# Performance work log

Measured on AMD Instinct MI355X. Metric: run time of the kernel, lower is better.

## Reference

```python
import jax, jax.numpy as jnp
import numpy as np
import math

B, S, H, NH, R = 1, 1024, 4096, 32, 16
HD = H // NH
BLOCK = 64
PRUNE_RATIO = 0.5
NF4_TABLE = jnp.array([
    -1.0, -0.6961928009986877, -0.5250730514526367, -0.39491748809814453,
    -0.28444138169288635, -0.18477343022823334, -0.09105003625154495, 0.0,
    0.07958029955625534, 0.16093020141124725, 0.24611230194568634,
    0.33791524171829224, 0.4407098591327667, 0.5626170039176941,
    0.7229568362236023, 1.0], dtype=jnp.float32)


def dequant_nf4(codes, absmax):
    # codes: [out,in] int4 values in [0,16); absmax: per-64-elem block scale
    vals = NF4_TABLE[codes.reshape(-1)]                 # [out*in]
    vals = vals.reshape(-1, BLOCK) * absmax[:, None]    # blockwise rescale
    return vals.reshape(codes.shape)                    # [out,in]


def setup_inputs() -> dict:
    key = jax.random.key(0)
    ks = jax.random.split(key, 32)
    d = {"x": jax.random.normal(ks[0], (B, S, H), dtype=jnp.float32)}
    i = 1
    for n in ("q", "k", "v", "o"):
        d[f"w_{n}_codes"] = jax.random.randint(ks[i], (H, H), 0, 16, dtype=jnp.int32); i += 1
        d[f"w_{n}_absmax"] = jax.random.uniform(ks[i], (H * H // BLOCK,), dtype=jnp.float32) * 0.06; i += 1
        d[f"b_{n}"] = jax.random.normal(ks[i], (H,), dtype=jnp.float32) * 0.01; i += 1
        d[f"w_{n}_lora_a"] = jax.random.normal(ks[i], (H, R), dtype=jnp.float32) * (1.0 / math.sqrt(H)); i += 1
        d[f"w_{n}_lora_b"] = jax.random.normal(ks[i], (R, H), dtype=jnp.float32) * 0.02; i += 1
    causal = jnp.tril(jnp.ones((S, S), dtype=bool))
    d["attention_mask"] = jnp.where(causal, 0.0, -1e9).astype(jnp.float32)[None, None]
    return d


def _proj(x, codes, absmax, b, la, lb):
    w = dequant_nf4(codes, absmax).T          # [in,out]
    main = x @ w + b
    lora_a = x @ la                            # [B,S,R]
    return main + lora_a @ lb, main, lora_a


def _kth_val(t, use_abs=True):
    flat = jnp.abs(t).ravel() if use_abs else t.ravel()
    k = int(t.size * PRUNE_RATIO)
    return jnp.sort(flat)[k - 1]


def reference(x, w_q_codes, w_q_absmax, b_q, w_q_lora_a, w_q_lora_b,
              w_k_codes, w_k_absmax, b_k, w_k_lora_a, w_k_lora_b,
              w_v_codes, w_v_absmax, b_v, w_v_lora_a, w_v_lora_b,
              w_o_codes, w_o_absmax, b_o, w_o_lora_a, w_o_lora_b,
              attention_mask):
    q, _, _ = _proj(x, w_q_codes, w_q_absmax, b_q, w_q_lora_a, w_q_lora_b)
    k, _, _ = _proj(x, w_k_codes, w_k_absmax, b_k, w_k_lora_a, w_k_lora_b)
    v, _, _ = _proj(x, w_v_codes, w_v_absmax, b_v, w_v_lora_a, w_v_lora_b)
    # [B,S,H] -> [B,NH,S,HD]
    qh = q.reshape(B, S, NH, HD).transpose(0, 2, 1, 3)
    kh = k.reshape(B, S, NH, HD).transpose(0, 2, 1, 3)
    vh = v.reshape(B, S, NH, HD).transpose(0, 2, 1, 3)
    s = jnp.einsum("bhqd,bhkd->bhqk", qh, kh) / math.sqrt(HD) + attention_mask
    a = jax.nn.softmax(s, axis=-1)
    o = jnp.einsum("bhqk,bhkd->bhqd", a, vh)
    o = o.transpose(0, 2, 1, 3).reshape(B, S, H)
    o_final, _, _ = _proj(o, w_o_codes, w_o_absmax, b_o, w_o_lora_a, w_o_lora_b)
    # iteration < 10 branch: magnitude-pruning thresholds via kth smallest value
    kth_vals = jnp.stack([
        _kth_val(x), _kth_val(qh), _kth_val(kh), _kth_val(vh),
        _kth_val(a, use_abs=False), _kth_val(o)])
    return o_final, kth_vals
```

## Files before the change

### kernel.cpp

```cpp
#include <hip/hip_runtime.h>

#define S_LEN  1024
#define H_DIM  4096
#define NHEAD  32
#define HEAD_D 128
#define RANK   16
#define KE3    4160
#define KEO    4128
#define TOTP   ((long)NHEAD * S_LEN * S_LEN)

typedef __bf16 bf16x8 __attribute__((ext_vector_type(8)));
typedef float  f32x4  __attribute__((ext_vector_type(4)));
typedef unsigned short ushort8v __attribute__((ext_vector_type(8)));

#define GLOAD_LDS16(g, l) __builtin_amdgcn_global_load_lds( \
    (const __attribute__((address_space(1))) unsigned int*)(g), \
    (__attribute__((address_space(3))) unsigned int*)(l), 16, 0, 0)

__device__ const float NF4_TAB[16] = {
    -1.0f, -0.6961928009986877f, -0.5250730514526367f, -0.39491748809814453f,
    -0.28444138169288635f, -0.18477343022823334f, -0.09105003625154495f, 0.0f,
    0.07958029955625534f, 0.16093020141124725f, 0.24611230194568634f,
    0.33791524171829224f, 0.4407098591327667f, 0.5626170039176941f,
    0.7229568362236023f, 1.0f};

__device__ __forceinline__ unsigned short f2bf(float f) {
    unsigned int u = __builtin_bit_cast(unsigned int, f);
    u = (u + 0x7FFFu + ((u >> 16) & 1u)) >> 16;
    return (unsigned short)u;
}

__device__ __forceinline__ float bf2f(unsigned short s) {
    return __builtin_bit_cast(float, (unsigned int)s << 16);
}

__device__ __forceinline__ void dequant_body(
    const int* __restrict__ codes, const float* __restrict__ absmax,
    unsigned short* __restrict__ out, long i, int ostride) {
    int4 c0 = *(const int4*)(codes + i);
    int4 c1 = *(const int4*)(codes + i + 4);
    float am = absmax[i >> 6];
    long orow = i >> 12;
    int  col  = (int)(i & 4095);
    ushort8v r;
    r[0] = f2bf(NF4_TAB[c0.x] * am);
    r[1] = f2bf(NF4_TAB[c0.y] * am);
    r[2] = f2bf(NF4_TAB[c0.z] * am);
    r[3] = f2bf(NF4_TAB[c0.w] * am);
    r[4] = f2bf(NF4_TAB[c1.x] * am);
    r[5] = f2bf(NF4_TAB[c1.y] * am);
    r[6] = f2bf(NF4_TAB[c1.z] * am);
    r[7] = f2bf(NF4_TAB[c1.w] * am);
    *(ushort8v*)(out + orow * ostride + col) = r;
}

__global__ __launch_bounds__(256) void prep_weights(
    const int* __restrict__ c0, const int* __restrict__ c1,
    const int* __restrict__ c2, const int* __restrict__ c3,
    const float* __restrict__ a0, const float* __restrict__ a1,
    const float* __restrict__ a2, const float* __restrict__ a3,
    const float* __restrict__ lb0, const float* __restrict__ lb1,
    const float* __restrict__ lb2, const float* __restrict__ lb3,
    const float* __restrict__ b0, const float* __restrict__ b1,
    const float* __restrict__ b2,
    unsigned short* __restrict__ wqkv, unsigned short* __restrict__ wo,
    float* __restrict__ bias3, unsigned int* __restrict__ hist, long n) {
    int p = blockIdx.y;
    long bx = blockIdx.x;
    int tid = threadIdx.x;
    if (bx < 8192) {
        const int* codes = (p == 0) ? c0 : (p == 1) ? c1 : (p == 2) ? c2 : c3;
        const float* am  = (p == 0) ? a0 : (p == 1) ? a1 : (p == 2) ? a2 : a3;
        long i = (bx * 256 + tid) * 8;
        if (i >= n) return;
        if (p < 3) dequant_body(codes, am, wqkv + (size_t)p * H_DIM * KE3, i, KE3);
        else       dequant_body(codes, am, wo, i, KEO);
        return;
    }
    if (p < 3) {
        long g = (bx - 8192) * 256 + tid;
        int row = (int)(g >> 6), c = (int)(g & 63);
        const float* lb = (p == 0) ? lb0 : (p == 1) ? lb1 : lb2;
        unsigned int r = (unsigned int)(c - 16 * p);
        float v = (r < 16u) ? lb[r * H_DIM + row] : 0.f;
        wqkv[(size_t)p * H_DIM * KE3 + (long)row * KE3 + 4096 + c] = f2bf(v);
        if (g < H_DIM) {
            const float* bp = (p == 0) ? b0 : (p == 1) ? b1 : b2;
            bias3[(size_t)p * H_DIM + g] = bp[g];
        }
        return;
    }
    if (bx < 8704) {
        long g = (bx - 8192) * 256 + tid;
        if (g >= (long)H_DIM * 32) return;
        int row = (int)(g >> 5), c = (int)(g & 31);
        float v = (c < 16) ? lb3[c * H_DIM + row] : 0.f;
        wo[(long)row * KEO + 4096 + c] = f2bf(v);
        return;
    }
    if (bx < 9088) {
        long g = (bx - 8704) * 256 + tid;
        if (g < 6 * 16384) hist[g] = 0u;
    }
}

__global__ __launch_bounds__(256) void cast_lora(
    const float* __restrict__ x, const float* __restrict__ la0,
    const float* __restrict__ la1, const float* __restrict__ la2,
    unsigned short* __restrict__ xb_ext) {
    __shared__ float xs[4096];
    int m = blockIdx.x, tid = threadIdx.x;
    const float* xr = x + (long)m * H_DIM;
    int c = tid * 16;
    float4 f0 = *(const float4*)(xr + c);
    float4 f1 = *(const float4*)(xr + c + 4);
    float4 f2 = *(const float4*)(xr + c + 8);
    float4 f3 = *(const float4*)(xr + c + 12);
    *(float4*)(xs + c)      = f0;
    *(float4*)(xs + c + 4)  = f1;
    *(float4*)(xs + c + 8)  = f2;
    *(float4*)(xs + c + 12) = f3;
    ushort8v r0, r1;
    r0[0] = f2bf(f0.x); r0[1] = f2bf(f0.y); r0[2] = f2bf(f0.z); r0[3] = f2bf(f0.w);
    r0[4] = f2bf(f1.x); r0[5] = f2bf(f1.y); r0[6] = f2bf(f1.z); r0[7] = f2bf(f1.w);
    r1[0] = f2bf(f2.x); r1[1] = f2bf(f2.y); r1[2] = f2bf(f2.z); r1[3] = f2bf(f2.w);
    r1[4] = f2bf(f3.x); r1[5] = f2bf(f3.y); r1[6] = f2bf(f3.z); r1[7] = f2bf(f3.w);
    unsigned short* orow = xb_ext + (long)m * KE3 + c;
    *(ushort8v*)orow = r0;
    *(ushort8v*)(orow + 8) = r1;
    __syncthreads();
    int w = tid >> 6, lane = tid & 63;
    if (w < 3) {
        const float* la = (w == 0) ? la0 : (w == 1) ? la1 : la2;
        float s[16];
#pragma unroll
        for (int r = 0; r < 16; ++r) s[r] = 0.f;
        for (int k = lane; k < H_DIM; k += 64) {
            float xv = xs[k];
            const float4* lr = (const float4*)(la + (long)k * RANK);
            float4 q0 = lr[0], q1 = lr[1], q2 = lr[2], q3 = lr[3];
            s[0] += xv * q0.x;  s[1] += xv * q0.y;  s[2] += xv * q0.z;  s[3] += xv * q0.w;
            s[4] += xv * q1.x;  s[5] += xv * q1.y;  s[6] += xv * q1.z;  s[7] += xv * q1.w;
            s[8] += xv * q2.x;  s[9] += xv * q2.y;  s[10] += xv * q2.z; s[11] += xv * q2.w;
            s[12] += xv * q3.x; s[13] += xv * q3.y; s[14] += xv * q3.z; s[15] += xv * q3.w;
        }
        for (int off = 32; off; off >>= 1)
#pragma unroll
            for (int r = 0; r < 16; ++r) s[r] += __shfl_xor(s[r], off);
        if (lane == 0)
#pragma unroll
            for (int r = 0; r < 16; ++r)
                xb_ext[(long)m * KE3 + 4096 + 16 * w + r] = f2bf(s[r]);
    }
}

__global__ void transpose_bf16_kernel(const unsigned short* __restrict__ v,
                                      unsigned short* __restrict__ vt) {
    __shared__ unsigned short tile[32][33];
    int c0 = blockIdx.x * 32, s0 = blockIdx.y * 32;
    int tx = threadIdx.x, ty = threadIdx.y;
    tile[ty][tx] = v[(long)(s0 + ty) * H_DIM + c0 + tx];
    __syncthreads();
    vt[(long)(c0 + ty) * S_LEN + s0 + tx] = tile[tx][ty];
}

__global__ __launch_bounds__(256) void lora_ao_kernel(
    unsigned short* __restrict__ ob_ext, const float* __restrict__ la) {
    int m = blockIdx.x;
    const unsigned short* xr = ob_ext + (long)m * KEO;
    int tid = threadIdx.x, lane = tid & 63, wid = tid >> 6;
    float s[4] = {0.f, 0.f, 0.f, 0.f};
    for (int k = lane; k < H_DIM; k += 64) {
        float xv = bf2f(xr[k]);
        const float* lr = la + (long)k * RANK + wid * 4;
        s[0] += xv * lr[0]; s[1] += xv * lr[1];
        s[2] += xv * lr[2]; s[3] += xv * lr[3];
    }
    for (int off = 32; off; off >>= 1)
        for (int r = 0; r < 4; ++r) s[r] += __shfl_down(s[r], off);
    if (lane == 0)
        for (int r = 0; r < 4; ++r)
            ob_ext[(long)m * KEO + 4096 + wid * 4 + r] = f2bf(s[r]);
}

__global__ __launch_bounds__(256) void gemm_nt(
    const unsigned short* __restrict__ A, const unsigned short* __restrict__ B,
    void* __restrict__ Cv, void* __restrict__ Cv2, const float* __restrict__ bias,
    int K, int lda, int ldb, int ldc,
    long strideA, long strideB, long strideC, float alpha, int mode, int obf) {
    int bm, bn;
    int k0s = 0, k0e = K;
    if (mode == 1) {
        int i = blockIdx.x;
        int tm = (int)((sqrtf(8.f * i + 1.f) - 1.f) * 0.5f);
        if ((tm + 1) * (tm + 2) / 2 <= i) tm++;
        if (tm * (tm + 1) / 2 > i) tm--;
        int tn = i - tm * (tm + 1) / 2;
        bm = tm * 128; bn = tn * 128;
    } else {
        bm = blockIdx.y * 128; bn = blockIdx.x * 128;
        if (mode == 2) { int kl = bm + 128; if (kl < k0e) k0e = kl; }
    }
    const unsigned short* Ab = A;
    const unsigned short* Bb = B;
    long coff = 0;
    void* Cuse = Cv;
    if (mode == 3) {
        int Kh = (K / 2) & ~31;
        k0s = blockIdx.z ? Kh : 0;
        k0e = blockIdx.z ? K : Kh;
        Cuse = blockIdx.z ? Cv2 : Cv;
    } else {
        Ab += (long)blockIdx.z * strideA;
        Bb += (long)blockIdx.z * strideB;
        coff = (long)blockIdx.z * strideC;
    }
    __shared__ unsigned short As[128][32];
    __shared__ unsigned short Bs[128][32];
    const int tid = threadIdx.x;
    const int lane = tid & 63, wid = tid >> 6;
    const int wm = (wid >> 1) * 64, wn = (wid & 1) * 64;
    const int sr = wid * 16 + (lane >> 2);
    const int sc = (lane & 3) * 8;
    const unsigned short* gA0 = Ab + (long)(bm + sr) * lda + sc;
    const unsigned short* gA1 = gA0 + (long)64 * lda;
    const unsigned short* gB0 = Bb + (long)(bn + sr) * ldb + sc;
    const unsigned short* gB1 = gB0 + (long)64 * ldb;
    unsigned short* lA0 = &As[wid * 16][0];
    unsigned short* lA1 = &As[64 + wid * 16][0];
    unsigned short* lB0 = &Bs[wid * 16][0];
    unsigned short* lB1 = &Bs[64 + wid * 16][0];
    f32x4 acc[4][4] = {};
    const int kq = (lane >> 4) * 8;
    const int rr = lane & 15;
    for (int k0 = k0s; k0 < k0e; k0 += 32) {
        GLOAD_LDS16(gA0 + k0, lA0);
        GLOAD_LDS16(gA1 + k0, lA1);
        GLOAD_LDS16(gB0 + k0, lB0);
        GLOAD_LDS16(gB1 + k0, lB1);
        __syncthreads();
        bf16x8 af[4], bfr[4];
        for (int i = 0; i < 4; ++i) {
            uint4 ta = *(const uint4*)&As[wm + i * 16 + rr][kq];
            uint4 tb = *(const uint4*)&Bs[wn + i * 16 + rr][kq];
            af[i]  = __builtin_bit_cast(bf16x8, ta);
            bfr[i] = __builtin_bit_cast(bf16x8, tb);
        }
        for (int i = 0; i < 4; ++i)
            for (int j = 0; j < 4; ++j)
                acc[i][j] = __builtin_amdgcn_mfma_f32_16x16x32_bf16(
                    af[i], bfr[j], acc[i][j], 0, 0, 0);
        __syncthreads();
    }
    const int cr = (lane >> 4) * 4;
    const int cc = lane & 15;
    float bv[4];
#pragma unroll
    for (int j = 0; j < 4; ++j)
        bv[j] = bias ? bias[(long)blockIdx.z * H_DIM + bn + wn + j * 16 + cc] : 0.f;
    if (obf) {
        unsigned short* Cb = (unsigned short*)Cuse + coff;
        for (int i = 0; i < 4; ++i)
            for (int j = 0; j < 4; ++j) {
                unsigned short* cp = Cb + (long)(bm + wm + i * 16 + cr) * ldc
                                        + (bn + wn + j * 16 + cc);
                for (int r = 0; r < 4; ++r)
                    cp[(long)r * ldc] = f2bf(acc[i][j][r] * alpha + bv[j]);
            }
    } else {
        float* Cb = (float*)Cuse + coff;
        for (int i = 0; i < 4; ++i)
            for (int j = 0; j < 4; ++j) {
                float* cp = Cb + (long)(bm + wm + i * 16 + cr) * ldc
                               + (bn + wn + j * 16 + cc);
                for (int r = 0; r < 4; ++r)
                    cp[(long)r * ldc] = acc[i][j][r] * alpha + bv[j];
            }
    }
}

__global__ __launch_bounds__(256) void combine_kernel(
    float* __restrict__ out, const float* __restrict__ part,
    const float* __restrict__ bias) {
    long idx = ((long)blockIdx.x * 256 + threadIdx.x) * 4;
    int n = (int)(idx & 4095);
    float4 o = *(float4*)(out + idx);
    float4 p = *(const float4*)(part + idx);
    float4 b = *(const float4*)(bias + n);
    o.x += p.x + b.x; o.y += p.y + b.y; o.z += p.z + b.z; o.w += p.w + b.w;
    *(float4*)(out + idx) = o;
}

__global__ __launch_bounds__(256) void softmax_causal(unsigned short* __restrict__ scores16) {
    int b = blockIdx.x;
    int h = b >> 9, pr = b & 511;
    int tid = threadIdx.x, lane = tid & 63, wid = tid >> 6;
    __shared__ float red[4], red2[4];
    for (int half = 0; half < 2; ++half) {
        int i = half ? (S_LEN - 1 - pr) : pr;
        unsigned short* row = scores16 + ((long)h * S_LEN + i) * S_LEN;
        int L = i + 1;
        float v[4];
        float mx = -1e30f;
        for (int t = 0; t < 4; ++t) {
            int j = tid + (t << 8);
            v[t] = (j < L) ? bf2f(row[j]) : -1e30f;
            mx = fmaxf(mx, v[t]);
        }
        for (int off = 32; off; off >>= 1) mx = fmaxf(mx, __shfl_xor(mx, off));
        if (lane == 0) red[wid] = mx;
        __syncthreads();
        mx = fmaxf(fmaxf(red[0], red[1]), fmaxf(red[2], red[3]));
        float e[4], sum = 0.f;
        for (int t = 0; t < 4; ++t) {
            int j = tid + (t << 8);
            e[t] = (j < L) ? __expf(v[t] - mx) : 0.f;
            sum += e[t];
        }
        for (int off = 32; off; off >>= 1) sum += __shfl_xor(sum, off);
        if (lane == 0) red2[wid] = sum;
        __syncthreads();
        sum = red2[0] + red2[1] + red2[2] + red2[3];
        float inv = 1.f / sum;
        for (int t = 0; t < 4; ++t) {
            int j = tid + (t << 8);
            row[j] = f2bf(e[t] * inv);
        }
        __syncthreads();
    }
}

__global__ __launch_bounds__(256, 2) void hist6(
    const float* __restrict__ x, const unsigned short* __restrict__ qkv,
    const unsigned short* __restrict__ ob, const unsigned short* __restrict__ P,
    unsigned int* __restrict__ hist) {
    __shared__ unsigned int lh[16384];
    const long SH = (long)S_LEN * H_DIM;
    int t = threadIdx.x;
    int b = blockIdx.x;
    int ten, b0, nblk;
    if (b < 256)      { ten = 0; b0 = 0;   nblk = 256; }
    else if (b < 384) { ten = 1; b0 = 256; nblk = 128; }
    else if (b < 512) { ten = 2; b0 = 384; nblk = 128; }
    else if (b < 640) { ten = 3; b0 = 512; nblk = 128; }
    else if (b < 768) { ten = 4; b0 = 640; nblk = 128; }
    else              { ten = 5; b0 = 768; nblk = 768; }
    unsigned int* gh = hist + (long)ten * 16384;
    for (int k = t; k < 16384; k += 256) lh[k] = 0u;
    __syncthreads();
    long i = (long)(b - b0) * 256 + t;
    long stride = (long)nblk * 256;
    if (ten == 0) {
        for (; i < SH / 4; i += stride) {
            float4 v = *(const float4*)(x + i * 4);
            unsigned int u0 = (__builtin_bit_cast(unsigned int, v.x) & 0x7FFFFFFFu) >> 16;
            unsigned int u1 = (__builtin_bit_cast(unsigned int, v.y) & 0x7FFFFFFFu) >> 16;
            unsigned int u2 = (__builtin_bit_cast(unsigned int, v.z) & 0x7FFFFFFFu) >> 16;
            unsigned int u3 = (__builtin_bit_cast(unsigned int, v.w) & 0x7FFFFFFFu) >> 16;
            atomicAdd(&lh[u0 < 16384u ? u0 : 16383u], 1u);
            atomicAdd(&lh[u1 < 16384u ? u1 : 16383u], 1u);
            atomicAdd(&lh[u2 < 16384u ? u2 : 16383u], 1u);
            atomicAdd(&lh[u3 < 16384u ? u3 : 16383u], 1u);
        }
    } else if (ten <= 3) {
        const unsigned short* src = qkv + (size_t)(ten - 1) * SH;
        for (; i < SH / 8; i += stride) {
            ushort8v v = ((const ushort8v*)src)[i];
#pragma unroll
            for (int j = 0; j < 8; ++j) {
                unsigned int u = v[j] & 0x7FFFu;
                atomicAdd(&lh[u < 16384u ? u : 16383u], 1u);
            }
        }
    } else if (ten == 4) {
        for (; i < SH / 8; i += stride) {
            long off = (i >> 9) * KEO + ((i & 511) << 3);
            ushort8v v = *(const ushort8v*)(ob + off);
#pragma unroll
            for (int j = 0; j < 8; ++j) {
                unsigned int u = v[j] & 0x7FFFu;
                atomicAdd(&lh[u < 16384u ? u : 16383u], 1u);
            }
        }
    } else {
        unsigned int zc = 0;
        for (; i < TOTP / 8; i += stride) {
            ushort8v v = ((const ushort8v*)P)[i];
#pragma unroll
            for (int j = 0; j < 8; ++j) {
                unsigned int bb = v[j];
                if (bb == 0) zc++;
                else atomicAdd(&lh[bb < 16384u ? bb : 16383u], 1u);
            }
        }
        if (zc) atomicAdd(&lh[0], zc);
    }
    __syncthreads();
    for (int k = t; k < 16384; k += 256) {
        unsigned int c = lh[k];
        if (c) atomicAdd(&gh[k], c);
    }
}

__global__ __launch_bounds__(256) void scan6(
    const unsigned int* __restrict__ hist, float* __restrict__ out_kth) {
    int ten = blockIdx.x;
    const unsigned int* h = hist + (long)ten * 16384;
    __shared__ unsigned int part[256];
    int t = threadIdx.x;
    unsigned int s = 0;
    for (int b = 0; b < 64; ++b) s += h[t * 64 + b];
    part[t] = s;
    __syncthreads();
    if (t == 0) {
        long k = (ten == 5) ? TOTP / 2 : (long)S_LEN * H_DIM / 2;
        long c = 0;
        int ch = 0;
        for (; ch < 256; ++ch) {
            if (c + (long)part[ch] >= k) break;
            c += part[ch];
        }
        int bin = ch * 64;
        for (;; ++bin) {
            unsigned int hv = h[bin];
            if (c + (long)hv >= k) break;
            c += hv;
        }
        int slot = (ten == 4) ? 5 : (ten == 5) ? 4 : ten;
        out_kth[slot] = __builtin_bit_cast(float, (unsigned int)bin << 16);
    }
}

extern "C" void kernel_launch(void* const* d_in, const int* in_sizes, int n_in,
                              void* d_out, int out_size, void* d_ws, size_t ws_size,
                              hipStream_t stream) {
    (void)in_sizes; (void)n_in; (void)out_size; (void)ws_size;
    const float* x = (const float*)d_in[0];
    const int*   wcodes[4] = {(const int*)d_in[1], (const int*)d_in[6],
                              (const int*)d_in[11], (const int*)d_in[16]};
    const float* wabs[4]   = {(const float*)d_in[2], (const float*)d_in[7],
                              (const float*)d_in[12], (const float*)d_in[17]};
    const float* bias[4]   = {(const float*)d_in[3], (const float*)d_in[8],
                              (const float*)d_in[13], (const float*)d_in[18]};
    const float* lA[4]     = {(const float*)d_in[4], (const float*)d_in[9],
                              (const float*)d_in[14], (const float*)d_in[19]};
    const float* lB[4]     = {(const float*)d_in[5], (const float*)d_in[10],
                              (const float*)d_in[15], (const float*)d_in[20]};

    char* wp = (char*)d_ws;
    auto alloc = [&](size_t bytes) {
        char* p = wp; wp += (bytes + 255) & ~(size_t)255; return p;
    };
    const size_t SH  = (size_t)S_LEN * H_DIM;
    const long   nW  = (long)H_DIM * H_DIM;
    unsigned short* xb_ext = (unsigned short*)alloc((size_t)S_LEN * KE3 * 2);
    unsigned short* qkvb   = (unsigned short*)alloc(3 * SH * 2);
    unsigned short* vT     = (unsigned short*)alloc(SH * 2);
    unsigned short* ob_ext = (unsigned short*)alloc((size_t)S_LEN * KEO * 2);
    unsigned short* Wd_ext = (unsigned short*)alloc((size_t)H_DIM * KEO * 2);
    float*        opart  = (float*)alloc(SH * 4);
    float*        bias3  = (float*)alloc(3 * H_DIM * 4);
    unsigned int* hist   = (unsigned int*)alloc(6 * 16384 * 4);
    char* bigbuf = alloc((size_t)3 * H_DIM * KE3 * 2);
    unsigned short* Wqkv_ext = (unsigned short*)bigbuf;
    unsigned short* scores16 = (unsigned short*)bigbuf;

    float* out_final = (float*)d_out;
    float* out_kth   = out_final + SH;

    unsigned short* qb = qkvb;
    unsigned short* kb = qkvb + SH;
    unsigned short* vb = qkvb + 2 * SH;

    prep_weights<<<dim3(9216, 4), 256, 0, stream>>>(
        wcodes[0], wcodes[1], wcodes[2], wcodes[3],
        wabs[0], wabs[1], wabs[2], wabs[3],
        lB[0], lB[1], lB[2], lB[3],
        bias[0], bias[1], bias[2],
        Wqkv_ext, Wd_ext, bias3, hist, nW);

    cast_lora<<<S_LEN, 256, 0, stream>>>(x, lA[0], lA[1], lA[2], xb_ext);

    gemm_nt<<<dim3(32, 8, 3), 256, 0, stream>>>(
        xb_ext, Wqkv_ext, qkvb, nullptr, bias3, KE3, KE3, KE3, H_DIM,
        0, (long)H_DIM * KE3, (long)SH, 1.0f, 0, 1);

    transpose_bf16_kernel<<<dim3(H_DIM / 32, S_LEN / 32), dim3(32, 32), 0, stream>>>(vb, vT);

    gemm_nt<<<dim3(36, 1, NHEAD), 256, 0, stream>>>(
        qb, kb, scores16, nullptr, nullptr, HEAD_D, H_DIM, H_DIM, S_LEN,
        128, 128, (long)S_LEN * S_LEN, 0.08838834764831845f, 1, 1);

    softmax_causal<<<NHEAD * S_LEN / 2, 256, 0, stream>>>(scores16);

    gemm_nt<<<dim3(1, 8, NHEAD), 256, 0, stream>>>(
        scores16, vT, ob_ext, nullptr, nullptr, S_LEN,
        S_LEN, S_LEN, KEO,
        (long)S_LEN * S_LEN, (long)HEAD_D * S_LEN, 128, 1.0f, 2, 1);

    lora_ao_kernel<<<S_LEN, 256, 0, stream>>>(ob_ext, lA[3]);

    gemm_nt<<<dim3(32, 8, 2), 256, 0, stream>>>(
        ob_ext, Wd_ext, out_final, opart, nullptr, KEO, KEO, KEO, H_DIM,
        0, 0, 0, 1.0f, 3, 0);

    combine_kernel<<<4096, 256, 0, stream>>>(out_final, opart, bias[3]);

    hist6<<<1536, 256, 0, stream>>>(x, qkvb, ob_ext, scores16, hist);
    scan6<<<6, 256, 0, stream>>>(hist, out_kth);
}
```

Measured before the change: 779.3 us.

## Fold V transpose into QK gemm, merge combine with scan, swap grid order

The standalone V transpose now runs inside the QK^T score gemm launch, in extra blocks (blockIdx.x >= 36) that tile-transpose V through shared memory while the other blocks compute scores. The combine and scan kernels become one finish kernel, and the gemm grid is reordered so blockIdx.x walks M tiles, which changes the block rasterisation and L2 reuse of weight tiles. The goal is fewer launches and some overlap of the transpose with score computation. The risk is that a few transpose blocks with 32 tiles each become stragglers in the attention gemm.

```diff
diff --git a/kernel.cpp b/kernel.cpp
--- a/kernel.cpp
+++ b/kernel.cpp
@@ -154,16 +154,6 @@
     }
 }
 
-__global__ void transpose_bf16_kernel(const unsigned short* __restrict__ v,
-                                      unsigned short* __restrict__ vt) {
-    __shared__ unsigned short tile[32][33];
-    int c0 = blockIdx.x * 32, s0 = blockIdx.y * 32;
-    int tx = threadIdx.x, ty = threadIdx.y;
-    tile[ty][tx] = v[(long)(s0 + ty) * H_DIM + c0 + tx];
-    __syncthreads();
-    vt[(long)(c0 + ty) * S_LEN + s0 + tx] = tile[tx][ty];
-}
-
 __global__ __launch_bounds__(256) void lora_ao_kernel(
     unsigned short* __restrict__ ob_ext, const float* __restrict__ la) {
     int m = blockIdx.x;
@@ -187,18 +177,38 @@
     const unsigned short* __restrict__ A, const unsigned short* __restrict__ B,
     void* __restrict__ Cv, void* __restrict__ Cv2, const float* __restrict__ bias,
     int K, int lda, int ldb, int ldc,
-    long strideA, long strideB, long strideC, float alpha, int mode, int obf) {
+    long strideA, long strideB, long strideC, float alpha, int mode, int obf,
+    const unsigned short* __restrict__ tsrc, unsigned short* __restrict__ tdst) {
+    __shared__ unsigned short As[128][32];
+    __shared__ unsigned short Bs[128][32];
+    const int tid = threadIdx.x;
     int bm, bn;
     int k0s = 0, k0e = K;
     if (mode == 1) {
         int i = blockIdx.x;
+        if (i >= 36) {
+            unsigned short (*tl)[33] = (unsigned short(*)[33])&As[0][0];
+            int tb = (i - 36) + 4 * blockIdx.z;
+            int tx = tid & 31, ty = tid >> 5;
+            for (int tile = tb; tile < 4096; tile += 128) {
+                int tc = tile & 127, ts = tile >> 7;
+                int c0 = tc * 32, s0 = ts * 32;
+                for (int j = 0; j < 32; j += 8)
+                    tl[ty + j][tx] = tsrc[(long)(s0 + ty + j) * H_DIM + c0 + tx];
+                __syncthreads();
+                for (int j = 0; j < 32; j += 8)
+                    tdst[(long)(c0 + ty + j) * S_LEN + s0 + tx] = tl[tx][ty + j];
+                __syncthreads();
+            }
+            return;
+        }
         int tm = (int)((sqrtf(8.f * i + 1.f) - 1.f) * 0.5f);
         if ((tm + 1) * (tm + 2) / 2 <= i) tm++;
         if (tm * (tm + 1) / 2 > i) tm--;
         int tn = i - tm * (tm + 1) / 2;
         bm = tm * 128; bn = tn * 128;
     } else {
-        bm = blockIdx.y * 128; bn = blockIdx.x * 128;
+        bm = blockIdx.x * 128; bn = blockIdx.y * 128;
         if (mode == 2) { int kl = bm + 128; if (kl < k0e) k0e = kl; }
     }
     const unsigned short* Ab = A;
@@ -215,9 +225,6 @@
         Bb += (long)blockIdx.z * strideB;
         coff = (long)blockIdx.z * strideC;
     }
-    __shared__ unsigned short As[128][32];
-    __shared__ unsigned short Bs[128][32];
-    const int tid = threadIdx.x;
     const int lane = tid & 63, wid = tid >> 6;
     const int wm = (wid >> 1) * 64, wn = (wid & 1) * 64;
     const int sr = wid * 16 + (lane >> 2);
@@ -277,18 +284,6 @@
                     cp[(long)r * ldc] = acc[i][j][r] * alpha + bv[j];
             }
     }
-}
-
-__global__ __launch_bounds__(256) void combine_kernel(
-    float* __restrict__ out, const float* __restrict__ part,
-    const float* __restrict__ bias) {
-    long idx = ((long)blockIdx.x * 256 + threadIdx.x) * 4;
-    int n = (int)(idx & 4095);
-    float4 o = *(float4*)(out + idx);
-    float4 p = *(const float4*)(part + idx);
-    float4 b = *(const float4*)(bias + n);
-    o.x += p.x + b.x; o.y += p.y + b.y; o.z += p.z + b.z; o.w += p.w + b.w;
-    *(float4*)(out + idx) = o;
 }
 
 __global__ __launch_bounds__(256) void softmax_causal(unsigned short* __restrict__ scores16) {
@@ -402,23 +397,36 @@
     }
 }
 
-__global__ __launch_bounds__(256) void scan6(
-    const unsigned int* __restrict__ hist, float* __restrict__ out_kth) {
-    int ten = blockIdx.x;
+__global__ __launch_bounds__(256) void finish_kernel(
+    float* __restrict__ out, const float* __restrict__ part,
+    const float* __restrict__ bias, const unsigned int* __restrict__ hist,
+    float* __restrict__ out_kth) {
+    int b = blockIdx.x;
+    int t = threadIdx.x;
+    if (b < 4096) {
+        long idx = ((long)b * 256 + t) * 4;
+        int n = (int)(idx & 4095);
+        float4 o = *(float4*)(out + idx);
+        float4 p = *(const float4*)(part + idx);
+        float4 bb = *(const float4*)(bias + n);
+        o.x += p.x + bb.x; o.y += p.y + bb.y; o.z += p.z + bb.z; o.w += p.w + bb.w;
+        *(float4*)(out + idx) = o;
+        return;
+    }
+    int ten = b - 4096;
     const unsigned int* h = hist + (long)ten * 16384;
-    __shared__ unsigned int part[256];
-    int t = threadIdx.x;
+    __shared__ unsigned int partl[256];
     unsigned int s = 0;
-    for (int b = 0; b < 64; ++b) s += h[t * 64 + b];
-    part[t] = s;
+    for (int bb = 0; bb < 64; ++bb) s += h[t * 64 + bb];
+    partl[t] = s;
     __syncthreads();
     if (t == 0) {
         long k = (ten == 5) ? TOTP / 2 : (long)S_LEN * H_DIM / 2;
         long c = 0;
         int ch = 0;
         for (; ch < 256; ++ch) {
-            if (c + (long)part[ch] >= k) break;
-            c += part[ch];
+            if (c + (long)partl[ch] >= k) break;
+            c += partl[ch];
         }
         int bin = ch * 64;
         for (;; ++bin) {
@@ -481,31 +489,28 @@
 
     cast_lora<<<S_LEN, 256, 0, stream>>>(x, lA[0], lA[1], lA[2], xb_ext);
 
-    gemm_nt<<<dim3(32, 8, 3), 256, 0, stream>>>(
+    gemm_nt<<<dim3(8, 32, 3), 256, 0, stream>>>(
         xb_ext, Wqkv_ext, qkvb, nullptr, bias3, KE3, KE3, KE3, H_DIM,
-        0, (long)H_DIM * KE3, (long)SH, 1.0f, 0, 1);
-
-    transpose_bf16_kernel<<<dim3(H_DIM / 32, S_LEN / 32), dim3(32, 32), 0, stream>>>(vb, vT);
-
-    gemm_nt<<<dim3(36, 1, NHEAD), 256, 0, stream>>>(
+        0, (long)H_DIM * KE3, (long)SH, 1.0f, 0, 1, nullptr, nullptr);
+
+    gemm_nt<<<dim3(40, 1, NHEAD), 256, 0, stream>>>(
         qb, kb, scores16, nullptr, nullptr, HEAD_D, H_DIM, H_DIM, S_LEN,
-        128, 128, (long)S_LEN * S_LEN, 0.08838834764831845f, 1, 1);
+        128, 128, (long)S_LEN * S_LEN, 0.08838834764831845f, 1, 1, vb, vT);
 
     softmax_causal<<<NHEAD * S_LEN / 2, 256, 0, stream>>>(scores16);
 
-    gemm_nt<<<dim3(1, 8, NHEAD), 256, 0, stream>>>(
+    gemm_nt<<<dim3(8, 1, NHEAD), 256, 0, stream>>>(
         scores16, vT, ob_ext, nullptr, nullptr, S_LEN,
         S_LEN, S_LEN, KEO,
-        (long)S_LEN * S_LEN, (long)HEAD_D * S_LEN, 128, 1.0f, 2, 1);
+        (long)S_LEN * S_LEN, (long)HEAD_D * S_LEN, 128, 1.0f, 2, 1, nullptr, nullptr);
 
     lora_ao_kernel<<<S_LEN, 256, 0, stream>>>(ob_ext, lA[3]);
 
-    gemm_nt<<<dim3(32, 8, 2), 256, 0, stream>>>(
+    gemm_nt<<<dim3(8, 32, 2), 256, 0, stream>>>(
         ob_ext, Wd_ext, out_final, opart, nullptr, KEO, KEO, KEO, H_DIM,
-        0, 0, 0, 1.0f, 3, 0);
-
-    combine_kernel<<<4096, 256, 0, stream>>>(out_final, opart, bias[3]);
+        0, 0, 0, 1.0f, 3, 0, nullptr, nullptr);
 
     hist6<<<1536, 256, 0, stream>>>(x, qkvb, ob_ext, scores16, hist);
-    scan6<<<6, 256, 0, stream>>>(hist, out_kth);
-}
+
+    finish_kernel<<<4102, 256, 0, stream>>>(out_final, opart, bias[3], hist, out_kth);
+}
```

After: 793.7 us. No clear change (+1.9%).
